# Kernel optimization log

Hardware: AMD Instinct MI355X
Metric: run time of the kernel (lower is better)

Reference implementation:

```python
import jax, jax.numpy as jnp
import numpy as np

TEMP1, TEMP2, TEMP3 = 4.0, 5.0, 10.0
NORM_EPS = 1e-12   # F.normalize eps
COS_EPS = 1e-8     # custom_cosine_similarity eps


def setup_inputs() -> dict:
    key = jax.random.key(0)
    k1, k2 = jax.random.split(key)
    vis_embeds = jax.random.normal(k1, (16, 16, 16, 16, 128), dtype=jnp.float32)
    txt_embeds = jax.random.normal(k2, (16, 64, 128), dtype=jnp.float32)
    return {"vis_embeds": vis_embeds, "txt_embeds": txt_embeds}


def reference(vis_embeds, txt_embeds):
    # vis_embeds: [bs, h, w, d, E]; txt_embeds: [bs, T, E] (uniform token_len)
    bs, h, w, d, E = vis_embeds.shape
    S = h * w * d
    # L2-normalize along embedding dim (F.normalize)
    vn = vis_embeds / jnp.clip(jnp.linalg.norm(vis_embeds, axis=-1, keepdims=True), NORM_EPS)
    vn = vn.reshape(bs, S, E)                      # context, flattened source
    tn = txt_embeds / jnp.clip(jnp.linalg.norm(txt_embeds, axis=-1, keepdims=True), NORM_EPS)
    # attention_fn, vectorized over the outer loop index i (txt sample):
    # attn0[i,b,s,t] = <context_b[s], query_i[t]>
    attn0 = jnp.einsum('bse,ite->ibst', vn, tn)    # [bs_txt, bs_vis, S, T]
    s1 = jax.nn.softmax(attn0, axis=-1)            # softmax over query tokens t
    a = jax.nn.softmax(TEMP1 * jnp.swapaxes(s1, -1, -2), axis=-1)  # [i,b,t,s], softmax over s
    # weighted context: [i,b,t,E]
    wc = jnp.einsum('ibts,bse->ibte', a, vn)
    # custom cosine similarity along E between txt tokens and weighted context
    num = jnp.einsum('ibte,ite->ibt', wc, tn)
    w1 = jnp.linalg.norm(tn, axis=-1)              # [i,t] (== 1 up to normalize eps)
    w2 = jnp.linalg.norm(wc, axis=-1)              # [i,b,t]
    cos = num / jnp.clip(w1[:, None, :] * w2, COS_EPS)
    # row_sim: mul temp2, exp, sum over tokens (agg='sum'), log
    row = jnp.log(jnp.sum(jnp.exp(TEMP2 * cos), axis=-1))  # [i_txt, b_vis]
    sims = row.T * TEMP3                           # [b_vis, i_txt] matches torch cat(dim=1)
    labels = jnp.arange(bs)
    logp0 = jax.nn.log_softmax(sims, axis=-1)
    logp1 = jax.nn.log_softmax(sims.T, axis=-1)
    loss0 = -jnp.mean(logp0[labels, labels])
    loss1 = -jnp.mean(logp1[labels, labels])
    loss = (loss0 + loss1) / 2.0
    # att_maps: for sample i the original keeps attn[i] -> diagonal of [i,b,...]
    att_maps = a[labels, labels].reshape(bs, -1, h, w, d)  # [bs, T, h, w, d]
    return loss, att_maps
```

## Files before the change

### kernel.cpp

```cpp
#include <hip/hip_runtime.h>

constexpr int BS = 16;
constexpr int S  = 4096;
constexpr int E  = 128;
constexpr int T  = 64;
constexpr int NSP = 4;
constexpr int SSEG = S / NSP;
constexpr int CH = 128;
constexpr int NCH = SSEG / CH;
constexpr int ETS = 136;
constexpr int TNS = 136;
constexpr int PTS = 72;

constexpr long VN_OFF  = 0;
constexpr long VNT_OFF = (long)BS * S * E;
constexpr long WS_P    = (long)BS * S * E;
constexpr long WS_SIMS = WS_P + (long)256 * NSP * 8192;

typedef __attribute__((ext_vector_type(8))) short bf16x8;
typedef __attribute__((ext_vector_type(4))) float f32x4;

__device__ __forceinline__ unsigned short f2bf(float x) {
    unsigned u = __float_as_uint(x);
    u += 0x7FFFu + ((u >> 16) & 1u);
    return (unsigned short)(u >> 16);
}
__device__ __forceinline__ float bf2f(unsigned short v) {
    return __uint_as_float(((unsigned)v) << 16);
}

__global__ __launch_bounds__(512, 4)
void prep_kernel(const float* __restrict__ vis, unsigned short* __restrict__ wsv)
{
    __shared__ unsigned short Lt[128 * PTS];
    const int tid  = threadIdx.x;
    const int b    = blockIdx.x >> 5;
    const int tile = blockIdx.x & 31;
    const int s0   = tile * 128;
    const float* visb = vis + ((long)b * S + s0) * E;
    unsigned short* vn  = wsv + VN_OFF  + ((long)b * S + s0) * E;
    unsigned short* vnT = wsv + VNT_OFF + (long)b * E * S;

#pragma unroll
    for (int half = 0; half < 2; ++half) {
        if (half) __syncthreads();
        {
            const int pp = tid >> 4, ee = tid & 15;
            const int r  = (half << 6) + (pp << 1);
            const float* rA = visb + (long)r * E + (ee << 1);
            float2 va[4], vb[4];
            float sa = 0.f, sb = 0.f;
#pragma unroll
            for (int k = 0; k < 4; ++k) {
                va[k] = *(const float2*)(rA + (k << 5));
                vb[k] = *(const float2*)(rA + E + (k << 5));
                sa = fmaf(va[k].x, va[k].x, fmaf(va[k].y, va[k].y, sa));
                sb = fmaf(vb[k].x, vb[k].x, fmaf(vb[k].y, vb[k].y, sb));
            }
            sa += __shfl_xor(sa, 1); sa += __shfl_xor(sa, 2);
            sa += __shfl_xor(sa, 4); sa += __shfl_xor(sa, 8);
            sb += __shfl_xor(sb, 1); sb += __shfl_xor(sb, 2);
            sb += __shfl_xor(sb, 4); sb += __shfl_xor(sb, 8);
            const float ia = 1.0f / fmaxf(sqrtf(sa), 1e-12f);
            const float ib = 1.0f / fmaxf(sqrtf(sb), 1e-12f);
            const long r0 = (long)r * E, r1 = r0 + E;
#pragma unroll
            for (int k = 0; k < 4; ++k) {
                const int e0 = (ee << 1) + (k << 5);
                const unsigned ax = f2bf(va[k].x * ia), ay = f2bf(va[k].y * ia);
                const unsigned bx = f2bf(vb[k].x * ib), by = f2bf(vb[k].y * ib);
                *(unsigned*)&Lt[e0 * PTS + (pp << 1)]       = ax | (bx << 16);
                *(unsigned*)&Lt[(e0 + 1) * PTS + (pp << 1)] = ay | (by << 16);
                *(unsigned*)&vn[r0 + e0] = ax | (ay << 16);
                *(unsigned*)&vn[r1 + e0] = bx | (by << 16);
            }
        }
        __syncthreads();
        {
            const int e = tid >> 2, sg = tid & 3;
#pragma unroll
            for (int j = 0; j < 2; ++j) {
                const bf16x8 v = *(const bf16x8*)&Lt[e * PTS + (sg << 4) + (j << 3)];
                *(bf16x8*)&vnT[(long)e * S + s0 + (half << 6) + (sg << 4) + (j << 3)] = v;
            }
        }
    }
}

__global__ __launch_bounds__(512, 4)
void clip_main_kernel(const unsigned short* __restrict__ wsv,
                      const float* __restrict__ txt,
                      float* __restrict__ d_out,
                      float* __restrict__ wsf)
{
    __shared__ unsigned short ET[T * ETS];
    __shared__ unsigned short tnL[T * TNS];

    const int tid = threadIdx.x;
    const int w   = tid >> 6;
    const int l   = tid & 63;
    const int cl  = l & 15;
    const int q   = l >> 4;
    const int b   = blockIdx.x & 15;
    const int i   = (blockIdx.x >> 4) & 15;
    const int qt  = blockIdx.x >> 8;
    const bool diag = (i == b);

    {
        const int r = tid >> 3, seg = tid & 7;
        const float* tp = txt + ((long)i * T + r) * E + (seg << 4);
        const float4 a0 = *(const float4*)(tp);
        const float4 a1 = *(const float4*)(tp + 4);
        const float4 a2 = *(const float4*)(tp + 8);
        const float4 a3 = *(const float4*)(tp + 12);
        float ssq = a0.x*a0.x + a0.y*a0.y + a0.z*a0.z + a0.w*a0.w
                  + a1.x*a1.x + a1.y*a1.y + a1.z*a1.z + a1.w*a1.w
                  + a2.x*a2.x + a2.y*a2.y + a2.z*a2.z + a2.w*a2.w
                  + a3.x*a3.x + a3.y*a3.y + a3.z*a3.z + a3.w*a3.w;
        ssq += __shfl_xor(ssq, 1); ssq += __shfl_xor(ssq, 2); ssq += __shfl_xor(ssq, 4);
        const float inv = 1.0f / fmaxf(sqrtf(ssq), 1e-12f);
        bf16x8 f0, f1;
        f0[0]=(short)f2bf(a0.x*inv); f0[1]=(short)f2bf(a0.y*inv);
        f0[2]=(short)f2bf(a0.z*inv); f0[3]=(short)f2bf(a0.w*inv);
        f0[4]=(short)f2bf(a1.x*inv); f0[5]=(short)f2bf(a1.y*inv);
        f0[6]=(short)f2bf(a1.z*inv); f0[7]=(short)f2bf(a1.w*inv);
        f1[0]=(short)f2bf(a2.x*inv); f1[1]=(short)f2bf(a2.y*inv);
        f1[2]=(short)f2bf(a2.z*inv); f1[3]=(short)f2bf(a2.w*inv);
        f1[4]=(short)f2bf(a3.x*inv); f1[5]=(short)f2bf(a3.y*inv);
        f1[6]=(short)f2bf(a3.z*inv); f1[7]=(short)f2bf(a3.w*inv);
        *(bf16x8*)&tnL[r * TNS + (seg << 4)]     = f0;
        *(bf16x8*)&tnL[r * TNS + (seg << 4) + 8] = f1;
    }
    __syncthreads();

    f32x4 acc2[4];
#pragma unroll
    for (int n = 0; n < 4; ++n) acc2[n] = (f32x4){0.f,0.f,0.f,0.f};

    const unsigned short* vnb  = wsv + VN_OFF  + (long)b * S * E;
    const unsigned short* vntb = wsv + VNT_OFF + (long)b * E * S;
    float* attb = d_out + 1 + (long)b * (long)T * S;

    for (int ch = 0; ch < NCH; ++ch) {
        const int s0 = qt * SSEG + ch * CH;

        bf16x8 Bf[4];
        {
            const unsigned short* r0 = vnb + (long)(s0 + (w << 4) + cl) * E + (q << 3);
#pragma unroll
            for (int kk = 0; kk < 4; ++kk) Bf[kk] = *(const bf16x8*)(r0 + (kk << 5));
        }

        {
            f32x4 acc1[4];
#pragma unroll
            for (int mt = 0; mt < 4; ++mt) acc1[mt] = (f32x4){0.f,0.f,0.f,0.f};
#pragma unroll
            for (int kk = 0; kk < 4; ++kk)
#pragma unroll
                for (int mt = 0; mt < 4; ++mt) {
                    const bf16x8 tA = *(const bf16x8*)&tnL[((mt << 4) + cl) * TNS + (kk << 5) + (q << 3)];
                    acc1[mt] = __builtin_amdgcn_mfma_f32_16x16x32_bf16(tA, Bf[kk], acc1[mt], 0, 0, 0);
                }
            float ex[4][4];
            float ssum = 0.f;
#pragma unroll
            for (int mt = 0; mt < 4; ++mt)
#pragma unroll
                for (int r = 0; r < 4; ++r) {
                    const float v = __expf(acc1[mt][r]);
                    ex[mt][r] = v; ssum += v;
                }
            ssum += __shfl_xor(ssum, 16);
            ssum += __shfl_xor(ssum, 32);
            const float csc = 4.0f / ssum;
            const int sloc = (w << 4) + cl;
#pragma unroll
            for (int mt = 0; mt < 4; ++mt)
#pragma unroll
                for (int r = 0; r < 4; ++r)
                    ET[((mt << 4) + (q << 2) + r) * ETS + sloc] = f2bf(__expf(ex[mt][r] * csc));
        }
        __syncthreads();

        {
            const unsigned short* ar = vntb + (long)((w << 4) + cl) * S + s0 + (q << 3);
#pragma unroll
            for (int kk2 = 0; kk2 < 4; ++kk2) {
                const bf16x8 aV = *(const bf16x8*)(ar + (kk2 << 5));
#pragma unroll
                for (int n = 0; n < 4; ++n) {
                    const bf16x8 bE = *(const bf16x8*)&ET[((n << 4) + cl) * ETS + (kk2 << 5) + (q << 3)];
                    acc2[n] = __builtin_amdgcn_mfma_f32_16x16x32_bf16(aV, bE, acc2[n], 0, 0, 0);
                }
            }
        }

        if (diag) {
            const int t = tid >> 3, sg = (tid & 7) << 4;
            float* ap = attb + (long)t * S + s0 + sg;
            const bf16x8 v0 = *(const bf16x8*)&ET[t * ETS + sg];
            const bf16x8 v1 = *(const bf16x8*)&ET[t * ETS + sg + 8];
#pragma unroll
            for (int j = 0; j < 8; ++j) {
                ap[j]     = bf2f((unsigned short)v0[j]);
                ap[8 + j] = bf2f((unsigned short)v1[j]);
            }
        }
        __syncthreads();
    }

    {
        float* pp = wsf + WS_P + ((long)(((i << 4) + b) << 2) + qt) * 8192;
#pragma unroll
        for (int n = 0; n < 4; ++n)
#pragma unroll
            for (int r = 0; r < 4; ++r)
                pp[((w << 4) + (q << 2) + r) * 64 + (n << 4) + cl] = acc2[n][r];
    }
}

__global__ __launch_bounds__(1024, 2)
void post_kernel(float* __restrict__ d_out, const float* __restrict__ txt,
                 float* __restrict__ wsf)
{
    const int tid = threadIdx.x;
    if (blockIdx.x < BS * BS) {
        __shared__ float sA[1024], sB[1024], sC[1024];
        const int pair = blockIdx.x;
        const int t = tid & 63, g = tid >> 6;
        const int i = pair >> 4, b = pair & 15;
        const float* p0 = wsf + WS_P + (long)pair * NSP * 8192;
        const float* tp = txt + ((long)i * T + t) * E + (g << 3);

        float ssq = 0.f, num = 0.f, w2 = 0.f;
#pragma unroll
        for (int e = 0; e < 8; ++e) {
            const float tv = tp[e];
            const int idx = ((g << 3) + e) * 64 + t;
            const float wc = p0[idx] + p0[idx + 8192] + p0[idx + 16384] + p0[idx + 24576];
            ssq = fmaf(tv, tv, ssq);
            num = fmaf(wc, tv, num);
            w2  = fmaf(wc, wc, w2);
        }
        sA[tid] = ssq; sB[tid] = num; sC[tid] = w2;
        __syncthreads();
        if (tid < 64) {
            float ss = 0.f, nm = 0.f, ww = 0.f;
#pragma unroll
            for (int k = 0; k < 16; ++k) {
                ss += sA[(k << 6) + tid];
                nm += sB[(k << 6) + tid];
                ww += sC[(k << 6) + tid];
            }
            const float cosv = (nm / fmaxf(sqrtf(ss), 1e-12f)) / fmaxf(sqrtf(ww), 1e-20f);
            float r = __expf(5.0f * cosv);
#pragma unroll
            for (int m = 1; m < 64; m <<= 1) r += __shfl_xor(r, m);
            if (tid == 0) wsf[WS_SIMS + (b << 4) + i] = 10.0f * logf(r);
        }
        return;
    }
    __shared__ float r16[16];
    const int bt = blockIdx.x - BS * BS;
    float4* p4 = (float4*)(d_out + 1 + (long)bt * 4096);
    float4 v = p4[tid];
    float s = v.x + v.y + v.z + v.w;
#pragma unroll
    for (int m = 1; m < 64; m <<= 1) s += __shfl_xor(s, m);
    if ((tid & 63) == 0) r16[tid >> 6] = s;
    __syncthreads();
    float tot = 0.f;
#pragma unroll
    for (int k = 0; k < 16; ++k) tot += r16[k];
    const float inv = 1.0f / tot;
    v.x *= inv; v.y *= inv; v.z *= inv; v.w *= inv;
    p4[tid] = v;
}

__global__ __launch_bounds__(256, 1)
void loss_kernel(const float* __restrict__ wsf, float* __restrict__ d_out)
{
    __shared__ float sm[16][17];
    __shared__ float red[16];
    const int tid = threadIdx.x;
    const int bb = tid >> 4, ii = tid & 15;
    const float x = wsf[WS_SIMS + bb * 16 + ii];
    sm[bb][ii] = x;
    float m = x;
#pragma unroll
    for (int msk = 1; msk < 16; msk <<= 1) m = fmaxf(m, __shfl_xor(m, msk));
    float s = __expf(x - m);
#pragma unroll
    for (int msk = 1; msk < 16; msk <<= 1) s += __shfl_xor(s, msk);
    const float lsm0 = x - m - logf(s);
    __syncthreads();
    const float y = sm[ii][bb];
    float m1 = y;
#pragma unroll
    for (int msk = 1; msk < 16; msk <<= 1) m1 = fmaxf(m1, __shfl_xor(m1, msk));
    float s1 = __expf(y - m1);
#pragma unroll
    for (int msk = 1; msk < 16; msk <<= 1) s1 += __shfl_xor(s1, msk);
    const float lsm1 = y - m1 - logf(s1);
    if (bb == ii) red[bb] = lsm0 + lsm1;
    __syncthreads();
    if (tid == 0) {
        float tot = 0.f;
#pragma unroll
        for (int k = 0; k < 16; ++k) tot += red[k];
        d_out[0] = -tot / 32.0f;
    }
}

extern "C" void kernel_launch(void* const* d_in, const int* in_sizes, int n_in,
                              void* d_out, int out_size, void* d_ws, size_t ws_size,
                              hipStream_t stream)
{
    const float* vis = (const float*)d_in[0];
    const float* txt = (const float*)d_in[1];
    float* out = (float*)d_out;
    unsigned short* wsv = (unsigned short*)d_ws;
    float* wsf = (float*)d_ws;

    hipLaunchKernelGGL(prep_kernel, dim3(512), dim3(512), 0, stream, vis, wsv);
    hipLaunchKernelGGL(clip_main_kernel, dim3(BS * BS * NSP), dim3(512), 0, stream,
                       wsv, txt, out, wsf);
    hipLaunchKernelGGL(post_kernel, dim3(BS * BS + BS * T), dim3(1024), 0, stream,
                       out, txt, wsf);
    hipLaunchKernelGGL(loss_kernel, dim3(1), dim3(256), 0, stream, wsf, out);
}
```

Before: 186.2 us.

## Halve main-kernel block size and chunk width, give each wave two E-subtiles

```diff
diff --git a/kernel.cpp b/kernel.cpp
--- a/kernel.cpp
+++ b/kernel.cpp
@@ -6,9 +6,9 @@
 constexpr int T  = 64;
 constexpr int NSP = 4;
 constexpr int SSEG = S / NSP;
-constexpr int CH = 128;
+constexpr int CH = 64;
 constexpr int NCH = SSEG / CH;
-constexpr int ETS = 136;
+constexpr int ETS = 72;
 constexpr int TNS = 136;
 constexpr int PTS = 72;
 
@@ -87,7 +87,7 @@
     }
 }
 
-__global__ __launch_bounds__(512, 4)
+__global__ __launch_bounds__(256, 6)
 void clip_main_kernel(const unsigned short* __restrict__ wsv,
                       const float* __restrict__ txt,
                       float* __restrict__ d_out,
@@ -107,35 +107,34 @@
     const bool diag = (i == b);
 
     {
-        const int r = tid >> 3, seg = tid & 7;
-        const float* tp = txt + ((long)i * T + r) * E + (seg << 4);
-        const float4 a0 = *(const float4*)(tp);
-        const float4 a1 = *(const float4*)(tp + 4);
-        const float4 a2 = *(const float4*)(tp + 8);
-        const float4 a3 = *(const float4*)(tp + 12);
-        float ssq = a0.x*a0.x + a0.y*a0.y + a0.z*a0.z + a0.w*a0.w
-                  + a1.x*a1.x + a1.y*a1.y + a1.z*a1.z + a1.w*a1.w
-                  + a2.x*a2.x + a2.y*a2.y + a2.z*a2.z + a2.w*a2.w
-                  + a3.x*a3.x + a3.y*a3.y + a3.z*a3.z + a3.w*a3.w;
-        ssq += __shfl_xor(ssq, 1); ssq += __shfl_xor(ssq, 2); ssq += __shfl_xor(ssq, 4);
+        const int r = tid >> 2, seg = tid & 3;
+        const float* tp = txt + ((long)i * T + r) * E + (seg << 5);
+        float4 a[8];
+        float ssq = 0.f;
+#pragma unroll
+        for (int k = 0; k < 8; ++k) {
+            a[k] = *(const float4*)(tp + (k << 2));
+            ssq += a[k].x*a[k].x + a[k].y*a[k].y + a[k].z*a[k].z + a[k].w*a[k].w;
+        }
+        ssq += __shfl_xor(ssq, 1); ssq += __shfl_xor(ssq, 2);
         const float inv = 1.0f / fmaxf(sqrtf(ssq), 1e-12f);
-        bf16x8 f0, f1;
-        f0[0]=(short)f2bf(a0.x*inv); f0[1]=(short)f2bf(a0.y*inv);
-        f0[2]=(short)f2bf(a0.z*inv); f0[3]=(short)f2bf(a0.w*inv);
-        f0[4]=(short)f2bf(a1.x*inv); f0[5]=(short)f2bf(a1.y*inv);
-        f0[6]=(short)f2bf(a1.z*inv); f0[7]=(short)f2bf(a1.w*inv);
-        f1[0]=(short)f2bf(a2.x*inv); f1[1]=(short)f2bf(a2.y*inv);
-        f1[2]=(short)f2bf(a2.z*inv); f1[3]=(short)f2bf(a2.w*inv);
-        f1[4]=(short)f2bf(a3.x*inv); f1[5]=(short)f2bf(a3.y*inv);
-        f1[6]=(short)f2bf(a3.z*inv); f1[7]=(short)f2bf(a3.w*inv);
-        *(bf16x8*)&tnL[r * TNS + (seg << 4)]     = f0;
-        *(bf16x8*)&tnL[r * TNS + (seg << 4) + 8] = f1;
+#pragma unroll
+        for (int k = 0; k < 8; k += 2) {
+            bf16x8 f;
+            f[0]=(short)f2bf(a[k].x*inv);   f[1]=(short)f2bf(a[k].y*inv);
+            f[2]=(short)f2bf(a[k].z*inv);   f[3]=(short)f2bf(a[k].w*inv);
+            f[4]=(short)f2bf(a[k+1].x*inv); f[5]=(short)f2bf(a[k+1].y*inv);
+            f[6]=(short)f2bf(a[k+1].z*inv); f[7]=(short)f2bf(a[k+1].w*inv);
+            *(bf16x8*)&tnL[r * TNS + (seg << 5) + (k << 2)] = f;
+        }
     }
     __syncthreads();
 
-    f32x4 acc2[4];
-#pragma unroll
-    for (int n = 0; n < 4; ++n) acc2[n] = (f32x4){0.f,0.f,0.f,0.f};
+    f32x4 acc2[2][4];
+#pragma unroll
+    for (int es = 0; es < 2; ++es)
+#pragma unroll
+        for (int n = 0; n < 4; ++n) acc2[es][n] = (f32x4){0.f,0.f,0.f,0.f};
 
     const unsigned short* vnb  = wsv + VN_OFF  + (long)b * S * E;
     const unsigned short* vntb = wsv + VNT_OFF + (long)b * E * S;
@@ -184,20 +183,23 @@
         __syncthreads();
 
         {
-            const unsigned short* ar = vntb + (long)((w << 4) + cl) * S + s0 + (q << 3);
-#pragma unroll
-            for (int kk2 = 0; kk2 < 4; ++kk2) {
-                const bf16x8 aV = *(const bf16x8*)(ar + (kk2 << 5));
-#pragma unroll
-                for (int n = 0; n < 4; ++n) {
-                    const bf16x8 bE = *(const bf16x8*)&ET[((n << 4) + cl) * ETS + (kk2 << 5) + (q << 3)];
-                    acc2[n] = __builtin_amdgcn_mfma_f32_16x16x32_bf16(aV, bE, acc2[n], 0, 0, 0);
+#pragma unroll
+            for (int es = 0; es < 2; ++es) {
+                const unsigned short* ar = vntb + (long)((w << 5) + (es << 4) + cl) * S + s0 + (q << 3);
+#pragma unroll
+                for (int kk2 = 0; kk2 < 2; ++kk2) {
+                    const bf16x8 aV = *(const bf16x8*)(ar + (kk2 << 5));
+#pragma unroll
+                    for (int n = 0; n < 4; ++n) {
+                        const bf16x8 bE = *(const bf16x8*)&ET[((n << 4) + cl) * ETS + (kk2 << 5) + (q << 3)];
+                        acc2[es][n] = __builtin_amdgcn_mfma_f32_16x16x32_bf16(aV, bE, acc2[es][n], 0, 0, 0);
+                    }
                 }
             }
         }
 
         if (diag) {
-            const int t = tid >> 3, sg = (tid & 7) << 4;
+            const int t = tid >> 2, sg = (tid & 3) << 4;
             float* ap = attb + (long)t * S + s0 + sg;
             const bf16x8 v0 = *(const bf16x8*)&ET[t * ETS + sg];
             const bf16x8 v1 = *(const bf16x8*)&ET[t * ETS + sg + 8];
@@ -213,10 +215,12 @@
     {
         float* pp = wsf + WS_P + ((long)(((i << 4) + b) << 2) + qt) * 8192;
 #pragma unroll
-        for (int n = 0; n < 4; ++n)
-#pragma unroll
-            for (int r = 0; r < 4; ++r)
-                pp[((w << 4) + (q << 2) + r) * 64 + (n << 4) + cl] = acc2[n][r];
+        for (int es = 0; es < 2; ++es)
+#pragma unroll
+            for (int n = 0; n < 4; ++n)
+#pragma unroll
+                for (int r = 0; r < 4; ++r)
+                    pp[((w << 5) + (es << 4) + (q << 2) + r) * 64 + (n << 4) + cl] = acc2[es][n][r];
     }
 }
 
@@ -324,7 +328,7 @@
     float* wsf = (float*)d_ws;
 
     hipLaunchKernelGGL(prep_kernel, dim3(512), dim3(512), 0, stream, vis, wsv);
-    hipLaunchKernelGGL(clip_main_kernel, dim3(BS * BS * NSP), dim3(512), 0, stream,
+    hipLaunchKernelGGL(clip_main_kernel, dim3(BS * BS * NSP), dim3(256), 0, stream,
                        wsv, txt, out, wsf);
     hipLaunchKernelGGL(post_kernel, dim3(BS * BS + BS * T), dim3(1024), 0, stream,
                        out, txt, wsf);
```

Result: slower. 201.2 us (+8.1%).
